# Performance work log

Measured on AMD Instinct MI355X. Metric: run time of the kernel, lower is better.

The kernel has to match this reference:

```python
import jax, jax.numpy as jnp
import numpy as np

B, S, D, H, DH, F = 4, 2048, 1024, 16, 64, 4096
EPS = 1e-5


def setup_inputs() -> dict:
    key = jax.random.key(0)
    ks = jax.random.split(key, 8)
    std = 0.02
    return {
        "src": jax.random.normal(ks[0], (B, S, D), dtype=jnp.float32),
        # per-head Q/K/V projections, stacked: [H, D, DH]
        "Wq": jax.random.normal(ks[1], (H, D, DH), dtype=jnp.float32) * std,
        "bq": jnp.zeros((H, DH), dtype=jnp.float32),
        "Wk": jax.random.normal(ks[2], (H, D, DH), dtype=jnp.float32) * std,
        "bk": jnp.zeros((H, DH), dtype=jnp.float32),
        "Wv": jax.random.normal(ks[3], (H, D, DH), dtype=jnp.float32) * std,
        "bv": jnp.zeros((H, DH), dtype=jnp.float32),
        "Wo": jax.random.normal(ks[4], (H * DH, D), dtype=jnp.float32) * std,
        "bo": jnp.zeros((D,), dtype=jnp.float32),
        "ln1_w": jnp.ones((D,), dtype=jnp.float32),
        "ln1_b": jnp.zeros((D,), dtype=jnp.float32),
        "W1": jax.random.normal(ks[5], (D, F), dtype=jnp.float32) * std,
        "b1": jnp.zeros((F,), dtype=jnp.float32),
        "W2": jax.random.normal(ks[6], (F, D), dtype=jnp.float32) * std,
        "b2": jnp.zeros((D,), dtype=jnp.float32),
        "ln2_w": jnp.ones((D,), dtype=jnp.float32),
        "ln2_b": jnp.zeros((D,), dtype=jnp.float32),
    }


def _layernorm(x, w, b):
    m = jnp.mean(x, axis=-1, keepdims=True)
    v = jnp.mean(jnp.square(x - m), axis=-1, keepdims=True)
    return (x - m) * jax.lax.rsqrt(v + EPS) * w + b


def reference(src, Wq, bq, Wk, bk, Wv, bv, Wo, bo, ln1_w, ln1_b, W1, b1, W2, b2, ln2_w, ln2_b):
    # Per-head projections, batched over heads: [B,H,S,DH]
    q = jnp.einsum('bsd,hde->bhse', src, Wq) + bq[None, :, None, :]
    k = jnp.einsum('bsd,hde->bhse', src, Wk) + bk[None, :, None, :]
    v = jnp.einsum('bsd,hde->bhse', src, Wv) + bv[None, :, None, :]
    scale = jnp.asarray(DH, src.dtype) ** 0.5
    scores = jnp.einsum('bhqe,bhke->bhqk', q, k) / scale  # [B,H,S,S]
    attn = jax.nn.softmax(scores, axis=-1)
    ctx = jnp.einsum('bhqk,bhke->bhqe', attn, v)  # [B,H,S,DH]
    # concat heads along feature dim (matches torch.cat over head outputs)
    ctx = ctx.transpose(0, 2, 1, 3).reshape(src.shape[0], src.shape[1], H * DH)
    attn_out = ctx @ Wo + bo
    x = _layernorm(src + attn_out, ln1_w, ln1_b)
    ffn = jax.nn.relu(x @ W1 + b1) @ W2 + b2
    return _layernorm(x + ffn, ln2_w, ln2_b)
```

## Files before the change

### kernel.cpp

```cpp
#include <hip/hip_runtime.h>
#include <stdint.h>


typedef unsigned short u16;
typedef __attribute__((ext_vector_type(8))) short short8;
typedef __attribute__((ext_vector_type(4))) float f32x4;

__device__ __forceinline__ u16 f2bf(float f) {
  union { float f; unsigned u; } v; v.f = f;
  unsigned r = (v.u + 0x7fffu + ((v.u >> 16) & 1u)) >> 16;
  return (u16)r;
}

__device__ __forceinline__ unsigned pack_trunc(float f0, float f1) {
  union { float f; unsigned u; } a, b;
  a.f = f0; b.f = f1;
  return __builtin_amdgcn_perm(b.u, a.u, 0x07060302u);
}

__device__ __forceinline__ void gl_lds16(const u16* g, u16* l) {
  __builtin_amdgcn_global_load_lds(
      (const __attribute__((address_space(1))) unsigned int*)g,
      (__attribute__((address_space(3))) unsigned int*)l, 16, 0, 0);
}


__global__ __launch_bounds__(256) void transpose_cast(const float* __restrict__ W,
                                                      u16* __restrict__ WT,
                                                      int K, int N) {
  __shared__ u16 T[64 * 72];
  const int tid = threadIdx.x;
  const long n0 = (long)blockIdx.x * 64, k0 = (long)blockIdx.y * 64;
#pragma unroll
  for (int i = 0; i < 4; i++) {
    int c = tid + i * 256;
    int kr = c >> 4, nc = (c & 15) * 4;
    float4 v = *(const float4*)(W + (k0 + kr) * N + n0 + nc);
    T[(nc + 0) * 72 + kr] = f2bf(v.x);
    T[(nc + 1) * 72 + kr] = f2bf(v.y);
    T[(nc + 2) * 72 + kr] = f2bf(v.z);
    T[(nc + 3) * 72 + kr] = f2bf(v.w);
  }
  __syncthreads();
#pragma unroll
  for (int i = 0; i < 2; i++) {
    int c = tid + i * 256;
    int nr = c >> 3, kc = (c & 7) * 8;
    *(uint4*)(WT + (n0 + nr) * K + k0 + kc) = *(const uint4*)(T + nr * 72 + kc);
  }
}

__global__ __launch_bounds__(256) void transpose_cast_qkv(const float* __restrict__ Wq,
                                                          const float* __restrict__ Wk,
                                                          const float* __restrict__ Wv,
                                                          u16* __restrict__ WT) {
  __shared__ u16 T[64 * 72];
  const int tid = threadIdx.x;
  const int n0 = blockIdx.x * 64, k0 = blockIdx.y * 64;
  const float* W = (n0 < 1024) ? Wq : (n0 < 2048 ? Wk : Wv);
  const int h = (n0 & 1023) >> 6;
#pragma unroll
  for (int i = 0; i < 4; i++) {
    int c = tid + i * 256;
    int kr = c >> 4, ec = (c & 15) * 4;
    float4 v = *(const float4*)(W + ((long)h * 1024 + k0 + kr) * 64 + ec);
    T[(ec + 0) * 72 + kr] = f2bf(v.x);
    T[(ec + 1) * 72 + kr] = f2bf(v.y);
    T[(ec + 2) * 72 + kr] = f2bf(v.z);
    T[(ec + 3) * 72 + kr] = f2bf(v.w);
  }
  __syncthreads();
#pragma unroll
  for (int i = 0; i < 2; i++) {
    int c = tid + i * 256;
    int nr = c >> 3, kc = (c & 7) * 8;
    *(uint4*)(WT + ((long)(n0 + nr)) * 1024 + k0 + kc) = *(const uint4*)(T + nr * 72 + kc);
  }
}

__global__ __launch_bounds__(256) void cast_bf16(const float* __restrict__ x, u16* __restrict__ y) {
  const long i = ((long)blockIdx.x * 256 + threadIdx.x) * 8;
  float4 a = *(const float4*)(x + i);
  float4 b = *(const float4*)(x + i + 4);
  uint4 o;
  o.x = (unsigned)f2bf(a.x) | ((unsigned)f2bf(a.y) << 16);
  o.y = (unsigned)f2bf(a.z) | ((unsigned)f2bf(a.w) << 16);
  o.z = (unsigned)f2bf(b.x) | ((unsigned)f2bf(b.y) << 16);
  o.w = (unsigned)f2bf(b.z) | ((unsigned)f2bf(b.w) << 16);
  *(uint4*)(y + i) = o;
}

__global__ __launch_bounds__(256) void build_bcat(const float* __restrict__ bq,
                                                  const float* __restrict__ bk,
                                                  const float* __restrict__ bv,
                                                  float* __restrict__ bcat) {
  int i = blockIdx.x * 256 + threadIdx.x;
  const float* s = (i < 1024) ? bq : (i < 2048 ? bk : bv);
  bcat[i] = s[i & 1023];
}

#define GEMM_PROLOGUE                                                              \
  __shared__ __align__(16) u16 As[2][128 * 32];                                    \
  __shared__ __align__(16) u16 Bs[2][128 * 32];                                    \
  const int tid = threadIdx.x;                                                     \
  const int wave = tid >> 6, lane = tid & 63, quad = lane >> 4, l15 = lane & 15;   \
  const int wm = (wave >> 1) * 64, wn = (wave & 1) * 64;                           \
  const int id = blockIdx.x, xcd = id & 7, ii = id >> 3;                           \
  const long m0 = (long)(xcd * 8 + (ii & 7)) * 128, n0 = (long)(ii >> 3) * 128;    \
  const u16* Ag = A + (m0 + (tid >> 2)) * K + (tid & 3) * 8;                       \
  const u16* Bg = B + (n0 + (tid >> 2)) * K + (tid & 3) * 8;                       \
  f32x4 acc[4][4] = {};                                                            \
  {                                                                                \
    gl_lds16(Ag, &As[0][tid * 8]);                                                 \
    gl_lds16(Ag + (long)64 * K, &As[0][tid * 8 + 2048]);                           \
    gl_lds16(Bg, &Bs[0][tid * 8]);                                                 \
    gl_lds16(Bg + (long)64 * K, &Bs[0][tid * 8 + 2048]);                           \
  }                                                                                \
  for (int k0 = 0; k0 < K; k0 += 32) {                                             \
    __syncthreads();         \
    const int cur = (k0 >> 5) & 1;                                                 \
    if (k0 + 32 < K) {                                                             \
      gl_lds16(Ag + k0 + 32, &As[cur ^ 1][tid * 8]);                               \
      gl_lds16(Ag + (long)64 * K + k0 + 32, &As[cur ^ 1][tid * 8 + 2048]);         \
      gl_lds16(Bg + k0 + 32, &Bs[cur ^ 1][tid * 8]);                               \
      gl_lds16(Bg + (long)64 * K + k0 + 32, &Bs[cur ^ 1][tid * 8 + 2048]);         \
    }                                                                              \
    short8 af[4], bfr[4];                                                          \
    _Pragma("unroll") for (int t = 0; t < 4; t++)                                  \
        af[t] = *(const short8*)(&As[cur][(wm + t * 16 + l15) * 32 + quad * 8]);   \
    _Pragma("unroll") for (int t = 0; t < 4; t++)                                  \
        bfr[t] = *(const short8*)(&Bs[cur][(wn + t * 16 + l15) * 32 + quad * 8]);  \
    _Pragma("unroll") for (int i = 0; i < 4; i++)                                  \
        _Pragma("unroll") for (int j = 0; j < 4; j++)                              \
            acc[i][j] = __builtin_amdgcn_mfma_f32_16x16x32_bf16(af[i], bfr[j],     \
                                                                acc[i][j], 0, 0, 0); \
  }

template <int MODE>
__global__ __launch_bounds__(256) void gemm_bt(const u16* __restrict__ A, const u16* __restrict__ B,
                                               const float* __restrict__ bias, void* __restrict__ Cout,
                                               int K, int N) {
  GEMM_PROLOGUE
#pragma unroll
  for (int i = 0; i < 4; i++) {
#pragma unroll
    for (int j = 0; j < 4; j++) {
      const long col = n0 + wn + j * 16 + l15;
      const float bb = bias[col];
      const long rowb = m0 + wm + i * 16 + quad * 4;
#pragma unroll
      for (int r = 0; r < 4; r++) {
        float v = acc[i][j][r] + bb;
        if (MODE == 2) v = fmaxf(v, 0.f);
        if (MODE == 0)
          ((float*)Cout)[(rowb + r) * N + col] = v;
        else
          ((u16*)Cout)[(rowb + r) * N + col] = f2bf(v);
      }
    }
  }
}

__global__ __launch_bounds__(256) void gemm_qkv(const u16* __restrict__ A, const u16* __restrict__ B,
                                                const float* __restrict__ bias,
                                                u16* __restrict__ QKb, u16* __restrict__ Vt, int K) {
  GEMM_PROLOGUE
#pragma unroll
  for (int i = 0; i < 4; i++) {
#pragma unroll
    for (int j = 0; j < 4; j++) {
      const int col0 = (int)n0 + wn + j * 16;
      const int col = col0 + l15;
      const float bb = bias[col];
      const long rowb = m0 + wm + i * 16 + quad * 4;
      if (col0 < 1024) {
#pragma unroll
        for (int r = 0; r < 4; r++)
          QKb[(rowb + r) * 2048 + col] = f2bf((acc[i][j][r] + bb) * 0.1803368801f);
      } else if (col0 < 2048) {
#pragma unroll
        for (int r = 0; r < 4; r++)
          QKb[(rowb + r) * 2048 + col] = f2bf(acc[i][j][r] + bb);
      } else {
        const int ec = col - 2048;
        const int bq = (int)(rowb >> 11), s = (int)(rowb & 2047);
        uint2 p;
        p.x = (unsigned)f2bf(acc[i][j][0] + bb) | ((unsigned)f2bf(acc[i][j][1] + bb) << 16);
        p.y = (unsigned)f2bf(acc[i][j][2] + bb) | ((unsigned)f2bf(acc[i][j][3] + bb) << 16);
        *(uint2*)(Vt + ((long)(bq * 16 + (ec >> 6)) * 64 + (ec & 63)) * 2048 + s) = p;
      }
    }
  }
}

#define PSLD 68

__device__ __forceinline__ void stage_tile(const u16* __restrict__ g, u16* __restrict__ lds, int tid) {
#pragma unroll
  for (int i = 0; i < 2; i++) {
    const int s = i * 256 + tid;
    const int r = s >> 3, cs = s & 7;
    const int c = cs ^ (r & 7);
    gl_lds16(g + (long)r * 2048 + c * 8, lds + s * 8);
  }
}
__device__ __forceinline__ short8 frag(const u16* __restrict__ buf, int row, int chunk) {
  const int slot = row * 8 + (chunk ^ (row & 7));
  return *(const short8*)(buf + slot * 8);
}

__global__ __launch_bounds__(256, 2) void flash_attn(const u16* __restrict__ QKb,
                                                     const u16* __restrict__ Vt,
                                                     u16* __restrict__ ctx) {
  __shared__ __align__(16) u16 Kbuf[2][4096];
  __shared__ __align__(16) u16 Vbuf[2][4096];
  __shared__ u16 Ps[8 * 16 * PSLD];
  const int tid = threadIdx.x, wave = tid >> 6, lane = tid & 63, quad = lane >> 4, l15 = lane & 15;
  const int bh = blockIdx.x, b = bh >> 4, h = bh & 15;
  const int qt = blockIdx.y;
  const u16* Qg = QKb + ((long)b * 2048 + qt * 256 + wave * 64) * 2048 + h * 64;
  const u16* Kg = QKb + ((long)b * 2048) * 2048 + 1024 + h * 64;
  const u16* Vg = Vt + (long)bh * 64 * 2048;

  short8 qf[4][2];
#pragma unroll
  for (int u = 0; u < 4; u++)
#pragma unroll
    for (int ks = 0; ks < 2; ks++)
      qf[u][ks] = *(const short8*)(Qg + (long)(u * 16 + l15) * 2048 + ks * 32 + quad * 8);

  f32x4 O[4][4] = {};
  f32x4 Os[4] = {};
  const short8 ones = {0x3F80, 0x3F80, 0x3F80, 0x3F80, 0x3F80, 0x3F80, 0x3F80, 0x3F80};
  u16* myP[2];
#pragma unroll
  for (int u = 0; u < 2; u++) myP[u] = Ps + ((wave * 2 + u) * 16 + l15) * PSLD;

  stage_tile(Kg, Kbuf[0], tid);
  stage_tile(Vg, Vbuf[0], tid);

  for (int kt = 0; kt < 32; kt++) {
    __syncthreads();
    if (kt < 31) {
      stage_tile(Kg + (long)(kt + 1) * 64 * 2048, Kbuf[(kt + 1) & 1], tid);
      stage_tile(Vg + (kt + 1) * 64, Vbuf[(kt + 1) & 1], tid);
    }
    const u16* Kb = Kbuf[kt & 1];
    const u16* Vb = Vbuf[kt & 1];

    short8 pf[4][2];
#pragma unroll
    for (int half = 0; half < 2; half++) {
      f32x4 S[2][4];
#pragma unroll
      for (int m = 0; m < 4; m++) {
        const short8 a0 = frag(Kb, m * 16 + l15, quad);
        const short8 a1 = frag(Kb, m * 16 + l15, 4 + quad);
#pragma unroll
        for (int uu = 0; uu < 2; uu++) {
          f32x4 s = {0.f, 0.f, 0.f, 0.f};
          s = __builtin_amdgcn_mfma_f32_16x16x32_bf16(a0, qf[half * 2 + uu][0], s, 0, 0, 0);
          s = __builtin_amdgcn_mfma_f32_16x16x32_bf16(a1, qf[half * 2 + uu][1], s, 0, 0, 0);
          S[uu][m] = s;
        }
      }

#pragma unroll
      for (int uu = 0; uu < 2; uu++)
#pragma unroll
        for (int m = 0; m < 4; m++) {
#pragma unroll
          for (int r = 0; r < 4; r++) S[uu][m][r] = __builtin_amdgcn_exp2f(S[uu][m][r]);
          uint2 p;
          p.x = pack_trunc(S[uu][m][0], S[uu][m][1]);
          p.y = pack_trunc(S[uu][m][2], S[uu][m][3]);
          *(uint2*)(myP[uu] + m * 16 + quad * 4) = p;
        }
#pragma unroll
      for (int uu = 0; uu < 2; uu++) {
        const int u = half * 2 + uu;
        pf[u][0] = *(const short8*)(myP[uu] + quad * 8);
        pf[u][1] = *(const short8*)(myP[uu] + 32 + quad * 8);
        Os[u] = __builtin_amdgcn_mfma_f32_16x16x32_bf16(ones, pf[u][0], Os[u], 0, 0, 0);
        Os[u] = __builtin_amdgcn_mfma_f32_16x16x32_bf16(ones, pf[u][1], Os[u], 0, 0, 0);
      }
    }

#pragma unroll
    for (int et = 0; et < 4; et++) {
      const short8 v0 = frag(Vb, et * 16 + l15, quad);
      const short8 v1 = frag(Vb, et * 16 + l15, 4 + quad);
#pragma unroll
      for (int u = 0; u < 4; u++) {
        O[u][et] = __builtin_amdgcn_mfma_f32_16x16x32_bf16(v0, pf[u][0], O[u][et], 0, 0, 0);
        O[u][et] = __builtin_amdgcn_mfma_f32_16x16x32_bf16(v1, pf[u][1], O[u][et], 0, 0, 0);
      }
    }
  }

#pragma unroll
  for (int u = 0; u < 4; u++) {
    const float inv = 1.f / Os[u][0];
    const long row = (long)b * 2048 + qt * 256 + wave * 64 + u * 16 + l15;
#pragma unroll
    for (int et = 0; et < 4; et++) {
      uint2 p;
      p.x = (unsigned)f2bf(O[u][et][0] * inv) | ((unsigned)f2bf(O[u][et][1] * inv) << 16);
      p.y = (unsigned)f2bf(O[u][et][2] * inv) | ((unsigned)f2bf(O[u][et][3] * inv) << 16);
      *(uint2*)(ctx + row * 1024 + h * 64 + et * 16 + quad * 4) = p;
    }
  }
}

template <bool WB>
__global__ __launch_bounds__(256) void add_ln(const float* __restrict__ a, const float* __restrict__ c,
                                              const float* __restrict__ w, const float* __restrict__ bias,
                                              float* __restrict__ xout, u16* __restrict__ xbf) {
  const int row = blockIdx.x, tid = threadIdx.x;
  const long off = (long)row * 1024 + tid * 4;
  float4 va = *(const float4*)(a + off);
  float4 vc = *(const float4*)(c + off);
  float4 s = {va.x + vc.x, va.y + vc.y, va.z + vc.z, va.w + vc.w};
  float sum = s.x + s.y + s.z + s.w;
  float sq = s.x * s.x + s.y * s.y + s.z * s.z + s.w * s.w;
#pragma unroll
  for (int o = 32; o > 0; o >>= 1) {
    sum += __shfl_xor(sum, o);
    sq += __shfl_xor(sq, o);
  }
  __shared__ float red[8];
  const int wave = tid >> 6;
  if ((tid & 63) == 0) { red[wave] = sum; red[wave + 4] = sq; }
  __syncthreads();
  sum = red[0] + red[1] + red[2] + red[3];
  sq = red[4] + red[5] + red[6] + red[7];
  const float mean = sum * (1.f / 1024.f);
  const float var = sq * (1.f / 1024.f) - mean * mean;
  const float rstd = rsqrtf(var + 1e-5f);
  float4 vw = *(const float4*)(w + tid * 4);
  float4 vb = *(const float4*)(bias + tid * 4);
  float4 y;
  y.x = (s.x - mean) * rstd * vw.x + vb.x;
  y.y = (s.y - mean) * rstd * vw.y + vb.y;
  y.z = (s.z - mean) * rstd * vw.z + vb.z;
  y.w = (s.w - mean) * rstd * vw.w + vb.w;
  *(float4*)(xout + off) = y;
  if (WB) {
    uint2 o2;
    o2.x = (unsigned)f2bf(y.x) | ((unsigned)f2bf(y.y) << 16);
    o2.y = (unsigned)f2bf(y.z) | ((unsigned)f2bf(y.w) << 16);
    *(uint2*)(xbf + off) = o2;
  }
}

extern "C" void kernel_launch(void* const* d_in, const int* in_sizes, int n_in,
                              void* d_out, int out_size, void* d_ws, size_t ws_size,
                              hipStream_t stream) {
  (void)in_sizes; (void)n_in; (void)out_size; (void)ws_size;
  const float* src = (const float*)d_in[0];
  const float* Wq = (const float*)d_in[1];
  const float* bq = (const float*)d_in[2];
  const float* Wk = (const float*)d_in[3];
  const float* bk = (const float*)d_in[4];
  const float* Wv = (const float*)d_in[5];
  const float* bv = (const float*)d_in[6];
  const float* Wo = (const float*)d_in[7];
  const float* bo = (const float*)d_in[8];
  const float* ln1w = (const float*)d_in[9];
  const float* ln1b = (const float*)d_in[10];
  const float* W1 = (const float*)d_in[11];
  const float* b1 = (const float*)d_in[12];
  const float* W2 = (const float*)d_in[13];
  const float* b2 = (const float*)d_in[14];
  const float* ln2w = (const float*)d_in[15];
  const float* ln2b = (const float*)d_in[16];

  char* ws = (char*)d_ws;
  u16* WqkvT = (u16*)(ws + 0);
  u16* WoT = (u16*)(ws + (6ul << 20));
  u16* W1T = (u16*)(ws + (8ul << 20));
  u16* W2T = (u16*)(ws + (16ul << 20));
  float* bcat = (float*)(ws + (24ul << 20));
  u16* srcb = (u16*)(ws + (25ul << 20));
  u16* QKb = (u16*)(ws + (41ul << 20));
  u16* Vt = (u16*)(ws + (73ul << 20));
  u16* ctxb = (u16*)(ws + (89ul << 20));
  float* x = (float*)(ws + (105ul << 20));
  u16* xb = (u16*)(ws + (137ul << 20));
  u16* hb = (u16*)(ws + (41ul << 20));
  float* out = (float*)d_out;

  transpose_cast_qkv<<<dim3(48, 16), 256, 0, stream>>>(Wq, Wk, Wv, WqkvT);
  transpose_cast<<<dim3(16, 16), 256, 0, stream>>>(Wo, WoT, 1024, 1024);
  transpose_cast<<<dim3(64, 16), 256, 0, stream>>>(W1, W1T, 1024, 4096);
  transpose_cast<<<dim3(16, 64), 256, 0, stream>>>(W2, W2T, 4096, 1024);
  cast_bf16<<<4096, 256, 0, stream>>>(src, srcb);
  build_bcat<<<12, 256, 0, stream>>>(bq, bk, bv, bcat);

  gemm_qkv<<<24 * 64, 256, 0, stream>>>(srcb, WqkvT, bcat, QKb, Vt, 1024);
  flash_attn<<<dim3(64, 8), 256, 0, stream>>>(QKb, Vt, ctxb);
  gemm_bt<0><<<8 * 64, 256, 0, stream>>>(ctxb, WoT, bo, out, 1024, 1024);
  add_ln<true><<<8192, 256, 0, stream>>>(src, out, ln1w, ln1b, x, xb);
  gemm_bt<2><<<32 * 64, 256, 0, stream>>>(xb, W1T, b1, hb, 1024, 4096);
  gemm_bt<0><<<8 * 64, 256, 0, stream>>>(hb, W2T, b2, out, 4096, 1024);
  add_ln<false><<<8192, 256, 0, stream>>>(x, out, ln2w, ln2b, out, nullptr);
}
```

Measured before the change: 562.0 us.

## Split flash attention blocks across eight waves with 32 query rows each

Flash attention blocks now use 512 threads, with each of 8 waves handling 32 query rows instead of 4 waves handling 64. This halves per-wave accumulator and Q fragment registers and spreads K/V tile staging over more threads, to raise occupancy and hide latency. In exchange, K/V fragments read from LDS are reused over fewer query tiles, which increases LDS traffic per MFMA.

```diff
diff --git a/kernel.cpp b/kernel.cpp
--- a/kernel.cpp
+++ b/kernel.cpp
@@ -195,21 +195,17 @@
 
 #define PSLD 68
 
-__device__ __forceinline__ void stage_tile(const u16* __restrict__ g, u16* __restrict__ lds, int tid) {
-#pragma unroll
-  for (int i = 0; i < 2; i++) {
-    const int s = i * 256 + tid;
-    const int r = s >> 3, cs = s & 7;
-    const int c = cs ^ (r & 7);
-    gl_lds16(g + (long)r * 2048 + c * 8, lds + s * 8);
-  }
+__device__ __forceinline__ void stage_tile512(const u16* __restrict__ g, u16* __restrict__ lds, int tid) {
+  const int r = tid >> 3, cs = tid & 7;
+  const int c = cs ^ (r & 7);
+  gl_lds16(g + (long)r * 2048 + c * 8, lds + tid * 8);
 }
 __device__ __forceinline__ short8 frag(const u16* __restrict__ buf, int row, int chunk) {
   const int slot = row * 8 + (chunk ^ (row & 7));
   return *(const short8*)(buf + slot * 8);
 }
 
-__global__ __launch_bounds__(256, 2) void flash_attn(const u16* __restrict__ QKb,
+__global__ __launch_bounds__(512, 4) void flash_attn(const u16* __restrict__ QKb,
                                                      const u16* __restrict__ Vt,
                                                      u16* __restrict__ ctx) {
   __shared__ __align__(16) u16 Kbuf[2][4096];
@@ -218,72 +214,69 @@
   const int tid = threadIdx.x, wave = tid >> 6, lane = tid & 63, quad = lane >> 4, l15 = lane & 15;
   const int bh = blockIdx.x, b = bh >> 4, h = bh & 15;
   const int qt = blockIdx.y;
-  const u16* Qg = QKb + ((long)b * 2048 + qt * 256 + wave * 64) * 2048 + h * 64;
+  const u16* Qg = QKb + ((long)b * 2048 + qt * 256 + wave * 32) * 2048 + h * 64;
   const u16* Kg = QKb + ((long)b * 2048) * 2048 + 1024 + h * 64;
   const u16* Vg = Vt + (long)bh * 64 * 2048;
 
-  short8 qf[4][2];
-#pragma unroll
-  for (int u = 0; u < 4; u++)
+  short8 qf[2][2];
+#pragma unroll
+  for (int u = 0; u < 2; u++)
 #pragma unroll
     for (int ks = 0; ks < 2; ks++)
       qf[u][ks] = *(const short8*)(Qg + (long)(u * 16 + l15) * 2048 + ks * 32 + quad * 8);
 
-  f32x4 O[4][4] = {};
-  f32x4 Os[4] = {};
+  f32x4 O[2][4] = {};
+  f32x4 Os[2] = {};
   const short8 ones = {0x3F80, 0x3F80, 0x3F80, 0x3F80, 0x3F80, 0x3F80, 0x3F80, 0x3F80};
-  u16* myP[2];
-#pragma unroll
-  for (int u = 0; u < 2; u++) myP[u] = Ps + ((wave * 2 + u) * 16 + l15) * PSLD;
-
-  stage_tile(Kg, Kbuf[0], tid);
-  stage_tile(Vg, Vbuf[0], tid);
+  u16* myP = Ps + (wave * 16 + l15) * PSLD;
+
+  stage_tile512(Kg, Kbuf[0], tid);
+  stage_tile512(Vg, Vbuf[0], tid);
 
   for (int kt = 0; kt < 32; kt++) {
     __syncthreads();
     if (kt < 31) {
-      stage_tile(Kg + (long)(kt + 1) * 64 * 2048, Kbuf[(kt + 1) & 1], tid);
-      stage_tile(Vg + (kt + 1) * 64, Vbuf[(kt + 1) & 1], tid);
+      stage_tile512(Kg + (long)(kt + 1) * 64 * 2048, Kbuf[(kt + 1) & 1], tid);
+      stage_tile512(Vg + (kt + 1) * 64, Vbuf[(kt + 1) & 1], tid);
     }
     const u16* Kb = Kbuf[kt & 1];
     const u16* Vb = Vbuf[kt & 1];
 
-    short8 pf[4][2];
-#pragma unroll
-    for (int half = 0; half < 2; half++) {
-      f32x4 S[2][4];
+    f32x4 S[2][4];
+#pragma unroll
+    for (int m = 0; m < 4; m++) {
+      const short8 a0 = frag(Kb, m * 16 + l15, quad);
+      const short8 a1 = frag(Kb, m * 16 + l15, 4 + quad);
+#pragma unroll
+      for (int u = 0; u < 2; u++) {
+        f32x4 s = {0.f, 0.f, 0.f, 0.f};
+        s = __builtin_amdgcn_mfma_f32_16x16x32_bf16(a0, qf[u][0], s, 0, 0, 0);
+        s = __builtin_amdgcn_mfma_f32_16x16x32_bf16(a1, qf[u][1], s, 0, 0, 0);
+        S[u][m] = s;
+      }
+    }
+
+#pragma unroll
+    for (int u = 0; u < 2; u++)
+#pragma unroll
+      for (int m = 0; m < 4; m++)
+#pragma unroll
+        for (int r = 0; r < 4; r++) S[u][m][r] = __builtin_amdgcn_exp2f(S[u][m][r]);
+
+    short8 pf[2][2];
+#pragma unroll
+    for (int u = 0; u < 2; u++) {
 #pragma unroll
       for (int m = 0; m < 4; m++) {
-        const short8 a0 = frag(Kb, m * 16 + l15, quad);
-        const short8 a1 = frag(Kb, m * 16 + l15, 4 + quad);
-#pragma unroll
-        for (int uu = 0; uu < 2; uu++) {
-          f32x4 s = {0.f, 0.f, 0.f, 0.f};
-          s = __builtin_amdgcn_mfma_f32_16x16x32_bf16(a0, qf[half * 2 + uu][0], s, 0, 0, 0);
-          s = __builtin_amdgcn_mfma_f32_16x16x32_bf16(a1, qf[half * 2 + uu][1], s, 0, 0, 0);
-          S[uu][m] = s;
-        }
+        uint2 p;
+        p.x = pack_trunc(S[u][m][0], S[u][m][1]);
+        p.y = pack_trunc(S[u][m][2], S[u][m][3]);
+        *(uint2*)(myP + m * 16 + quad * 4) = p;
       }
-
-#pragma unroll
-      for (int uu = 0; uu < 2; uu++)
-#pragma unroll
-        for (int m = 0; m < 4; m++) {
-#pragma unroll
-          for (int r = 0; r < 4; r++) S[uu][m][r] = __builtin_amdgcn_exp2f(S[uu][m][r]);
-          uint2 p;
-          p.x = pack_trunc(S[uu][m][0], S[uu][m][1]);
-          p.y = pack_trunc(S[uu][m][2], S[uu][m][3]);
-          *(uint2*)(myP[uu] + m * 16 + quad * 4) = p;
-        }
-#pragma unroll
-      for (int uu = 0; uu < 2; uu++) {
-        const int u = half * 2 + uu;
-        pf[u][0] = *(const short8*)(myP[uu] + quad * 8);
-        pf[u][1] = *(const short8*)(myP[uu] + 32 + quad * 8);
-        Os[u] = __builtin_amdgcn_mfma_f32_16x16x32_bf16(ones, pf[u][0], Os[u], 0, 0, 0);
-        Os[u] = __builtin_amdgcn_mfma_f32_16x16x32_bf16(ones, pf[u][1], Os[u], 0, 0, 0);
-      }
+      pf[u][0] = *(const short8*)(myP + quad * 8);
+      pf[u][1] = *(const short8*)(myP + 32 + quad * 8);
+      Os[u] = __builtin_amdgcn_mfma_f32_16x16x32_bf16(ones, pf[u][0], Os[u], 0, 0, 0);
+      Os[u] = __builtin_amdgcn_mfma_f32_16x16x32_bf16(ones, pf[u][1], Os[u], 0, 0, 0);
     }
 
 #pragma unroll
@@ -291,7 +284,7 @@
       const short8 v0 = frag(Vb, et * 16 + l15, quad);
       const short8 v1 = frag(Vb, et * 16 + l15, 4 + quad);
 #pragma unroll
-      for (int u = 0; u < 4; u++) {
+      for (int u = 0; u < 2; u++) {
         O[u][et] = __builtin_amdgcn_mfma_f32_16x16x32_bf16(v0, pf[u][0], O[u][et], 0, 0, 0);
         O[u][et] = __builtin_amdgcn_mfma_f32_16x16x32_bf16(v1, pf[u][1], O[u][et], 0, 0, 0);
       }
@@ -299,9 +292,9 @@
   }
 
 #pragma unroll
-  for (int u = 0; u < 4; u++) {
+  for (int u = 0; u < 2; u++) {
     const float inv = 1.f / Os[u][0];
-    const long row = (long)b * 2048 + qt * 256 + wave * 64 + u * 16 + l15;
+    const long row = (long)b * 2048 + qt * 256 + wave * 32 + u * 16 + l15;
 #pragma unroll
     for (int et = 0; et < 4; et++) {
       uint2 p;
@@ -398,7 +391,7 @@
   build_bcat<<<12, 256, 0, stream>>>(bq, bk, bv, bcat);
 
   gemm_qkv<<<24 * 64, 256, 0, stream>>>(srcb, WqkvT, bcat, QKb, Vt, 1024);
-  flash_attn<<<dim3(64, 8), 256, 0, stream>>>(QKb, Vt, ctxb);
+  flash_attn<<<dim3(64, 8), 512, 0, stream>>>(QKb, Vt, ctxb);
   gemm_bt<0><<<8 * 64, 256, 0, stream>>>(ctxb, WoT, bo, out, 1024, 1024);
   add_ln<true><<<8192, 256, 0, stream>>>(src, out, ln1w, ln1b, x, xb);
   gemm_bt<2><<<32 * 64, 256, 0, stream>>>(xb, W1T, b1, hb, 1024, 4096);
```

Result: no change. 557.2 us (-0.8%).

## Rewrite flash attention with 32x32x16 MFMA and register-resident P via permlane swap

Applied to the files above, without the earlier changes.

Switches the attention kernel from 16x16x32 to 32x32x16 bf16 MFMA tiles. The exponentiated score tile is converted to the P operand in registers with v_cvt_pk_bf16_f32 and v_permlane32_swap, which removes the LDS round-trip through the Ps buffer. The row sum is now accumulated in VALU adds plus one cross-half shuffle instead of extra MFMAs against a ones vector. This cuts LDS traffic and MFMA count in the inner loop, at the cost of more registers per accumulator, and it relies on gfx950-specific instructions plus a correct lane mapping for the operand layout.

```diff
diff --git a/kernel.cpp b/kernel.cpp
--- a/kernel.cpp
+++ b/kernel.cpp
@@ -5,6 +5,7 @@
 typedef unsigned short u16;
 typedef __attribute__((ext_vector_type(8))) short short8;
 typedef __attribute__((ext_vector_type(4))) float f32x4;
+typedef __attribute__((ext_vector_type(16))) float f32x16;
 
 __device__ __forceinline__ u16 f2bf(float f) {
   union { float f; unsigned u; } v; v.f = f;
@@ -12,16 +13,19 @@
   return (u16)r;
 }
 
-__device__ __forceinline__ unsigned pack_trunc(float f0, float f1) {
-  union { float f; unsigned u; } a, b;
-  a.f = f0; b.f = f1;
-  return __builtin_amdgcn_perm(b.u, a.u, 0x07060302u);
-}
-
 __device__ __forceinline__ void gl_lds16(const u16* g, u16* l) {
   __builtin_amdgcn_global_load_lds(
       (const __attribute__((address_space(1))) unsigned int*)g,
       (__attribute__((address_space(3))) unsigned int*)l, 16, 0, 0);
+}
+
+__device__ __forceinline__ unsigned cvtpk(float lo, float hi) {
+  unsigned r;
+  asm("v_cvt_pk_bf16_f32 %0, %1, %2" : "=v"(r) : "v"(lo), "v"(hi));
+  return r;
+}
+__device__ __forceinline__ void pl32_swap(unsigned& a, unsigned& b) {
+  asm("v_permlane32_swap_b32 %0, %1" : "+v"(a), "+v"(b));
 }
 
 
@@ -193,7 +197,6 @@
   }
 }
 
-#define PSLD 68
 
 __device__ __forceinline__ void stage_tile(const u16* __restrict__ g, u16* __restrict__ lds, int tid) {
 #pragma unroll
@@ -214,27 +217,24 @@
                                                      u16* __restrict__ ctx) {
   __shared__ __align__(16) u16 Kbuf[2][4096];
   __shared__ __align__(16) u16 Vbuf[2][4096];
-  __shared__ u16 Ps[8 * 16 * PSLD];
-  const int tid = threadIdx.x, wave = tid >> 6, lane = tid & 63, quad = lane >> 4, l15 = lane & 15;
+  const int tid = threadIdx.x, wave = tid >> 6, lane = tid & 63;
+  const int l31 = lane & 31, hi = lane >> 5;
   const int bh = blockIdx.x, b = bh >> 4, h = bh & 15;
   const int qt = blockIdx.y;
-  const u16* Qg = QKb + ((long)b * 2048 + qt * 256 + wave * 64) * 2048 + h * 64;
+  const long qbase = (long)b * 2048 + qt * 256 + wave * 64;
+  const u16* Qg = QKb + qbase * 2048 + h * 64;
   const u16* Kg = QKb + ((long)b * 2048) * 2048 + 1024 + h * 64;
   const u16* Vg = Vt + (long)bh * 64 * 2048;
 
-  short8 qf[4][2];
-#pragma unroll
-  for (int u = 0; u < 4; u++)
-#pragma unroll
-    for (int ks = 0; ks < 2; ks++)
-      qf[u][ks] = *(const short8*)(Qg + (long)(u * 16 + l15) * 2048 + ks * 32 + quad * 8);
-
-  f32x4 O[4][4] = {};
-  f32x4 Os[4] = {};
-  const short8 ones = {0x3F80, 0x3F80, 0x3F80, 0x3F80, 0x3F80, 0x3F80, 0x3F80, 0x3F80};
-  u16* myP[2];
-#pragma unroll
-  for (int u = 0; u < 2; u++) myP[u] = Ps + ((wave * 2 + u) * 16 + l15) * PSLD;
+  short8 qf[2][4];
+#pragma unroll
+  for (int j = 0; j < 2; j++)
+#pragma unroll
+    for (int ks = 0; ks < 4; ks++)
+      qf[j][ks] = *(const short8*)(Qg + (long)(j * 32 + l31) * 2048 + ks * 16 + hi * 8);
+
+  f32x16 O[2][2] = {};
+  float rs[2] = {0.f, 0.f};
 
   stage_tile(Kg, Kbuf[0], tid);
   stage_tile(Vg, Vbuf[0], tid);
@@ -248,67 +248,73 @@
     const u16* Kb = Kbuf[kt & 1];
     const u16* Vb = Vbuf[kt & 1];
 
-    short8 pf[4][2];
-#pragma unroll
-    for (int half = 0; half < 2; half++) {
-      f32x4 S[2][4];
-#pragma unroll
-      for (int m = 0; m < 4; m++) {
-        const short8 a0 = frag(Kb, m * 16 + l15, quad);
-        const short8 a1 = frag(Kb, m * 16 + l15, 4 + quad);
-#pragma unroll
-        for (int uu = 0; uu < 2; uu++) {
-          f32x4 s = {0.f, 0.f, 0.f, 0.f};
-          s = __builtin_amdgcn_mfma_f32_16x16x32_bf16(a0, qf[half * 2 + uu][0], s, 0, 0, 0);
-          s = __builtin_amdgcn_mfma_f32_16x16x32_bf16(a1, qf[half * 2 + uu][1], s, 0, 0, 0);
-          S[uu][m] = s;
-        }
+#pragma unroll
+    for (int m = 0; m < 2; m++) {
+      short8 ak[4];
+#pragma unroll
+      for (int ks = 0; ks < 4; ks++) ak[ks] = frag(Kb, m * 32 + l31, ks * 2 + hi);
+      f32x16 S[2] = {};
+#pragma unroll
+      for (int ks = 0; ks < 4; ks++)
+#pragma unroll
+        for (int j = 0; j < 2; j++)
+          S[j] = __builtin_amdgcn_mfma_f32_32x32x16_bf16(ak[ks], qf[j][ks], S[j], 0, 0, 0);
+
+      short8 pf[2][2];
+#pragma unroll
+      for (int j = 0; j < 2; j++) {
+#pragma unroll
+        for (int r = 0; r < 16; r++) S[j][r] = __builtin_amdgcn_exp2f(S[j][r]);
+        rs[j] += ((S[j][0] + S[j][1]) + (S[j][2] + S[j][3])) +
+                 ((S[j][4] + S[j][5]) + (S[j][6] + S[j][7])) +
+                 ((S[j][8] + S[j][9]) + (S[j][10] + S[j][11])) +
+                 ((S[j][12] + S[j][13]) + (S[j][14] + S[j][15]));
+        unsigned w0 = cvtpk(S[j][0], S[j][1]), w1 = cvtpk(S[j][2], S[j][3]);
+        unsigned w2 = cvtpk(S[j][4], S[j][5]), w3 = cvtpk(S[j][6], S[j][7]);
+        unsigned w4 = cvtpk(S[j][8], S[j][9]), w5 = cvtpk(S[j][10], S[j][11]);
+        unsigned w6 = cvtpk(S[j][12], S[j][13]), w7 = cvtpk(S[j][14], S[j][15]);
+        pl32_swap(w2, w0); pl32_swap(w3, w1);
+        pl32_swap(w6, w4); pl32_swap(w7, w5);
+        union { unsigned u[4]; short8 s8; } f0, f1;
+        f0.u[0] = w0; f0.u[1] = w1; f0.u[2] = w2; f0.u[3] = w3;
+        f1.u[0] = w4; f1.u[1] = w5; f1.u[2] = w6; f1.u[3] = w7;
+        pf[j][0] = f0.s8; pf[j][1] = f1.s8;
       }
 
 #pragma unroll
-      for (int uu = 0; uu < 2; uu++)
-#pragma unroll
-        for (int m = 0; m < 4; m++) {
-#pragma unroll
-          for (int r = 0; r < 4; r++) S[uu][m][r] = __builtin_amdgcn_exp2f(S[uu][m][r]);
-          uint2 p;
-          p.x = pack_trunc(S[uu][m][0], S[uu][m][1]);
-          p.y = pack_trunc(S[uu][m][2], S[uu][m][3]);
-          *(uint2*)(myP[uu] + m * 16 + quad * 4) = p;
-        }
-#pragma unroll
-      for (int uu = 0; uu < 2; uu++) {
-        const int u = half * 2 + uu;
-        pf[u][0] = *(const short8*)(myP[uu] + quad * 8);
-        pf[u][1] = *(const short8*)(myP[uu] + 32 + quad * 8);
-        Os[u] = __builtin_amdgcn_mfma_f32_16x16x32_bf16(ones, pf[u][0], Os[u], 0, 0, 0);
-        Os[u] = __builtin_amdgcn_mfma_f32_16x16x32_bf16(ones, pf[u][1], Os[u], 0, 0, 0);
+      for (int et = 0; et < 2; et++) {
+        short8 av[2];
+#pragma unroll
+        for (int ks2 = 0; ks2 < 2; ks2++)
+          av[ks2] = frag(Vb, et * 32 + l31, m * 4 + ks2 * 2 + hi);
+#pragma unroll
+        for (int j = 0; j < 2; j++)
+#pragma unroll
+          for (int ks2 = 0; ks2 < 2; ks2++)
+            O[et][j] = __builtin_amdgcn_mfma_f32_32x32x16_bf16(av[ks2], pf[j][ks2],
+                                                               O[et][j], 0, 0, 0);
       }
     }
-
-#pragma unroll
-    for (int et = 0; et < 4; et++) {
-      const short8 v0 = frag(Vb, et * 16 + l15, quad);
-      const short8 v1 = frag(Vb, et * 16 + l15, 4 + quad);
-#pragma unroll
-      for (int u = 0; u < 4; u++) {
-        O[u][et] = __builtin_amdgcn_mfma_f32_16x16x32_bf16(v0, pf[u][0], O[u][et], 0, 0, 0);
-        O[u][et] = __builtin_amdgcn_mfma_f32_16x16x32_bf16(v1, pf[u][1], O[u][et], 0, 0, 0);
+  }
+
+#pragma unroll
+  for (int j = 0; j < 2; j++) rs[j] += __shfl_xor(rs[j], 32);
+#pragma unroll
+  for (int j = 0; j < 2; j++) {
+    const float inv = 1.f / rs[j];
+    const long row = qbase + j * 32 + l31;
+#pragma unroll
+    for (int et = 0; et < 2; et++)
+#pragma unroll
+      for (int g = 0; g < 4; g++) {
+        const int e0 = et * 32 + g * 8 + hi * 4;
+        uint2 p;
+        p.x = (unsigned)f2bf(O[et][j][g * 4 + 0] * inv) |
+              ((unsigned)f2bf(O[et][j][g * 4 + 1] * inv) << 16);
+        p.y = (unsigned)f2bf(O[et][j][g * 4 + 2] * inv) |
+              ((unsigned)f2bf(O[et][j][g * 4 + 3] * inv) << 16);
+        *(uint2*)(ctx + row * 1024 + h * 64 + e0) = p;
       }
-    }
-  }
-
-#pragma unroll
-  for (int u = 0; u < 4; u++) {
-    const float inv = 1.f / Os[u][0];
-    const long row = (long)b * 2048 + qt * 256 + wave * 64 + u * 16 + l15;
-#pragma unroll
-    for (int et = 0; et < 4; et++) {
-      uint2 p;
-      p.x = (unsigned)f2bf(O[u][et][0] * inv) | ((unsigned)f2bf(O[u][et][1] * inv) << 16);
-      p.y = (unsigned)f2bf(O[u][et][2] * inv) | ((unsigned)f2bf(O[u][et][3] * inv) << 16);
-      *(uint2*)(ctx + row * 1024 + h * 64 + et * 16 + quad * 4) = p;
-    }
   }
 }
 
```

Result: faster. 514.3 us (-8.5%).
